# Optimization experiments

Measured on AMD Instinct MI355X. Metric: run time of the kernel, lower is better.

The kernel has to match this reference:

```python
import jax, jax.numpy as jnp
import numpy as np

B, N, QD = 2, 4096, 1024
CD = 1024
H, DH = 8, 64
INNER = H * DH  # 512


def setup_inputs() -> dict:
    key = jax.random.key(0)
    ks = jax.random.split(key, 10)
    s = lambda d: (1.0 / np.sqrt(d)).astype(np.float32)
    return {
        "x": jax.random.normal(ks[0], (B, N, QD), dtype=jnp.float32),
        "context": jax.random.normal(ks[1], (B, N, CD), dtype=jnp.float32),
        "mask": jax.random.randint(ks[2], (B, N + 1), 0, 2) > 0,
        # weights stored as [in, out] (y = x @ W), matching torch Linear math
        "Wq": jax.random.normal(ks[3], (QD, INNER), dtype=jnp.float32) * s(QD),
        "Wk": jax.random.normal(ks[4], (CD, INNER), dtype=jnp.float32) * s(CD),
        "Wv": jax.random.normal(ks[5], (CD, INNER), dtype=jnp.float32) * s(CD),
        "Wk_bg": jax.random.normal(ks[6], (QD, INNER), dtype=jnp.float32) * s(QD),
        "Wv_bg": jax.random.normal(ks[7], (QD, INNER), dtype=jnp.float32) * s(QD),
        "Wout": jax.random.normal(ks[8], (INNER, QD), dtype=jnp.float32) * s(INNER),
        "b_out": jax.random.normal(ks[9], (QD,), dtype=jnp.float32) * 0.01,
    }


def reference(x, context, mask, Wq, Wk, Wv, Wk_bg, Wv_bg, Wout, b_out):
    b, n, _ = x.shape
    scale = DH ** -0.5

    q = x @ Wq                                             # [b, n, inner]
    pooled_x = jax.lax.stop_gradient(jnp.mean(x, axis=1, keepdims=True))  # [b, 1, qd]
    k = jnp.concatenate([context @ Wk, pooled_x @ Wk_bg], axis=1)  # [b, n+1, inner]
    v = jnp.concatenate([context @ Wv, pooled_x @ Wv_bg], axis=1)  # [b, n+1, inner]

    split = lambda t: t.reshape(b, t.shape[1], H, DH).transpose(0, 2, 1, 3)  # b h j d
    qh, kh, vh = split(q), split(k), split(v)

    sim = jnp.einsum('bhid,bhjd->bhij', qh, kh) * scale     # [b, h, n, n+1]
    neg = -jnp.finfo(sim.dtype).max
    sim = jnp.where(mask[:, None, None, :], sim, neg)
    attn = jax.nn.softmax(sim, axis=-1)
    out = jnp.einsum('bhij,bhjd->bhid', attn, vh)           # [b, h, n, d]
    out = out.transpose(0, 2, 1, 3).reshape(b, n, INNER)    # [b, n, inner]
    return out @ Wout + b_out                                # dropout p=0 -> identity
```

## Files before the change

### kernel.cpp

```cpp
#include <hip/hip_runtime.h>
#include <stdint.h>

#define N_TOK 4096
#define QDIM  1024
#define CDIM  1024
#define NH    8
#define DH    64
#define INNER 512
#define BATCH 2
#define N1    4097
#define N1P   4128
#define NJB   129
#define VROWS 80
#define KTILE_SH 2048
#define VTILE_SH 2560

typedef __attribute__((ext_vector_type(8))) short short8;
typedef __attribute__((ext_vector_type(4))) float f32x4;
typedef __attribute__((ext_vector_type(4))) uint32_t u32x4;

__device__ __forceinline__ short f2bf(float f) {
    union { float f; uint32_t u; } x; x.f = f;
    uint32_t r = x.u + 0x7fffu + ((x.u >> 16) & 1u);
    return (short)(r >> 16);
}

__device__ __forceinline__ void async_copy16(void* lds, const void* g) {
    __builtin_amdgcn_global_load_lds(
        (const __attribute__((address_space(1))) void*)g,
        (__attribute__((address_space(3))) void*)lds, 16, 0, 0);
}

__global__ __launch_bounds__(256) void cast2_bf16_kernel(
        const float* __restrict__ a, const float* __restrict__ b,
        short* __restrict__ da, short* __restrict__ db, int n4) {
    int i = blockIdx.x * 256 + threadIdx.x;
    bool first = i < n4;
    const float* s = first ? a : b;
    short* d = first ? da : db;
    int j = first ? i : i - n4;
    float4 v = ((const float4*)s)[j];
    ((short4*)d)[j] = make_short4(f2bf(v.x), f2bf(v.y), f2bf(v.z), f2bf(v.w));
}

__global__ __launch_bounds__(256) void transpose_cast4_kernel(
        const float* __restrict__ Wq, const float* __restrict__ Wk,
        const float* __restrict__ Wv, const float* __restrict__ Wout,
        short* __restrict__ Wqt, short* __restrict__ Wkvt, short* __restrict__ Wot,
        float scale_q) {
    __shared__ float tile[32][33];
    int z = blockIdx.y;
    const float* W; short* Wt; int K, N; float scale = 1.f;
    if (z == 0)      { W = Wq;   Wt = Wqt;  K = QDIM;  N = INNER; scale = scale_q; }
    else if (z == 1) { W = Wk;   Wt = Wkvt; K = CDIM;  N = INNER; }
    else if (z == 2) { W = Wv;   Wt = Wkvt + (size_t)INNER * CDIM; K = CDIM; N = INNER; }
    else             { W = Wout; Wt = Wot;  K = INNER; N = QDIM; }
    int ntn = N >> 5;
    int bid = blockIdx.x;
    int n0 = (bid & (ntn - 1)) * 32, k0 = (bid / ntn) * 32;
    int tx = threadIdx.x & 31, ty = threadIdx.x >> 5;
    for (int r = ty; r < 32; r += 8)
        tile[r][tx] = W[(size_t)(k0 + r) * N + n0 + tx];
    __syncthreads();
    for (int r = ty; r < 32; r += 8)
        Wt[(size_t)(n0 + r) * K + k0 + tx] = f2bf(tile[tx][r] * scale);
}

__global__ __launch_bounds__(256) void pool_partial_kernel(
        const float* __restrict__ x, float* __restrict__ part) {
    int b = blockIdx.y, c = blockIdx.x;
    int t = threadIdx.x;
    float s0 = 0.f, s1 = 0.f, s2 = 0.f, s3 = 0.f;
    const float* xp = x + ((size_t)b * N_TOK + c * 128) * QDIM;
    for (int n = 0; n < 128; n++) {
        const float* row = xp + (size_t)n * QDIM;
        s0 += row[t];
        s1 += row[256 + t];
        s2 += row[512 + t];
        s3 += row[768 + t];
    }
    float* pp = part + ((size_t)b * 32 + c) * QDIM;
    pp[t] = s0; pp[256 + t] = s1; pp[512 + t] = s2; pp[768 + t] = s3;
}

__global__ __launch_bounds__(256) void bg_kernel(
        const float* __restrict__ part, const float* __restrict__ Wkbg,
        const float* __restrict__ Wvbg, short* __restrict__ kb, short* __restrict__ vb) {
    int b = blockIdx.x, jb = blockIdx.y, t = threadIdx.x;
    __shared__ float pooled[QDIM];
    for (int d = t; d < QDIM; d += 256) {
        float s = 0.f;
        for (int c = 0; c < 32; c++) s += part[((size_t)b * 32 + c) * QDIM + d];
        pooled[d] = s * (1.f / (float)N_TOK);
    }
    __syncthreads();
    int flat = jb * 256 + t;
    int matv = flat >> 9;
    int o = flat & 511;
    const float* W = matv ? Wvbg : Wkbg;
    float s = 0.f;
    for (int k = 0; k < QDIM; k++) s += pooled[k] * W[(size_t)k * INNER + o];
    int h = o >> 6, d = o & 63;
    if (matv) {
        vb[(((size_t)(b * NH + h)) * N1P + N_TOK) * DH + d] = f2bf(s);
    } else {
        kb[((size_t)(b * NH + h)) * NJB * KTILE_SH + 128 * KTILE_SH
           + (d >> 5) * 1024 + (d & 31)] = f2bf(s);
    }
    if (jb == 0) {
        for (int idx = t; idx < NH * 31 * DH; idx += 256) {
            int h2 = idx / (31 * DH);
            int r2 = idx % (31 * DH);
            int rr = 1 + r2 / DH;
            int d2 = r2 % DH;
            kb[((size_t)(b * NH + h2)) * NJB * KTILE_SH + 128 * KTILE_SH
               + (d2 >> 5) * 1024 + rr * 32 + (d2 & 31)] = 0;
        }
    }
}

__global__ __launch_bounds__(256) void transpose_v_kernel(
        const short* __restrict__ vin, short* __restrict__ vout,
        const int* __restrict__ mask) {
    __shared__ short tile[32][65];
    __shared__ int mloc[32];
    int bh = blockIdx.z, b = bh >> 3;
    int j0 = blockIdx.x * 32, jb = blockIdx.x;
    int tx = threadIdx.x & 63, ty = threadIdx.x >> 6;
    const short* src = vin + (size_t)bh * N1P * DH;
    for (int r = ty; r < 32; r += 4)
        tile[r][tx] = src[(size_t)(j0 + r) * DH + tx];
    if (threadIdx.x < 32) {
        int j = j0 + threadIdx.x;
        mloc[threadIdx.x] = (j < N1) ? mask[b * N1 + j] : 0;
    }
    __syncthreads();
    int tp = threadIdx.x & 31, dy = threadIdx.x >> 5;
    int s = (tp >> 3) * 4 + (tp & 3) + ((tp >> 2) & 1) * 16;
    bool mk = mloc[s] != 0;
    short* dst = vout + ((size_t)bh * NJB + jb) * VTILE_SH;
    for (int d = dy; d < DH; d += 8) {
        int swz = (((tp >> 3) ^ ((d >> 1) & 3)) << 3) | (tp & 7);
        dst[d * 32 + swz] = mk ? tile[s][d] : (short)0;
    }
    if (dy == 0) dst[64 * 32 + tp] = mk ? (short)0x3F80 : (short)0;
    if (dy == 1)
        for (int d = 65; d < 80; d++) dst[d * 32 + tp] = 0;
}

__global__ __launch_bounds__(256) void qkv_gemm_kernel(
        const short* __restrict__ x_bf, const short* __restrict__ c_bf,
        const short* __restrict__ Wqt, const short* __restrict__ Wkvt,
        short* __restrict__ q_bf, short* __restrict__ k_bf, short* __restrict__ v_tmp) {
    __shared__ short As[128 * 32];
    __shared__ short Bs[128 * 32];
    const int t = threadIdx.x;
    const int lane = t & 63, w = t >> 6;
    const int wr = w >> 1, wc = w & 1;
    const int lo = lane & 15, g = lane >> 4;
    const int arow = lane >> 2;
    const int ac8 = (lane & 3) * 8;

    const short *A, *W;
    int m0, n0, which;
    int bid = blockIdx.x;
    if (bid < 256) { A = x_bf; W = Wqt;  m0 = (bid >> 2) * 128; n0 = (bid & 3) * 128; which = 0; }
    else { int i = bid - 256; A = c_bf; W = Wkvt; m0 = (i >> 3) * 128; n0 = (i & 7) * 128;
           which = (n0 < 512) ? 1 : 2; }

    f32x4 acc[4][4] = {};
    for (int k0 = 0; k0 < 1024; k0 += 32) {
        for (int q = 0; q < 2; q++) {
            int seg = w * 2 + q;
            async_copy16(&As[seg * 512], A + (size_t)(m0 + seg * 16 + arow) * 1024 + k0 + ac8);
            async_copy16(&Bs[seg * 512], W + (size_t)(n0 + seg * 16 + arow) * 1024 + k0 + ac8);
        }
        __syncthreads();
        short8 af[4], bfv[4];
        #pragma unroll
        for (int i = 0; i < 4; i++)
            af[i] = *(const short8*)&As[(wr * 64 + i * 16 + lo) * 32 + g * 8];
        #pragma unroll
        for (int j = 0; j < 4; j++)
            bfv[j] = *(const short8*)&Bs[(wc * 64 + j * 16 + lo) * 32 + g * 8];
        #pragma unroll
        for (int i = 0; i < 4; i++)
            #pragma unroll
            for (int j = 0; j < 4; j++)
                acc[i][j] = __builtin_amdgcn_mfma_f32_16x16x32_bf16(af[i], bfv[j], acc[i][j], 0, 0, 0);
        __syncthreads();
    }

    if (which == 0) {
        #pragma unroll
        for (int i = 0; i < 4; i++)
            #pragma unroll
            for (int j = 0; j < 4; j++) {
                int row = m0 + wr * 64 + i * 16 + g * 4;
                int col0 = n0 + wc * 64 + j * 16 + lo;
                int h = col0 >> 6, d = col0 & 63;
                f32x4 v = acc[i][j];
                #pragma unroll
                for (int r = 0; r < 4; r++) {
                    int m = row + r;
                    int b = m >> 12, ii = m & 4095;
                    q_bf[(((size_t)(b * NH + h)) * N_TOK + ii) * DH + d] = f2bf(v[r]);
                }
            }
    } else if (which == 1) {
        #pragma unroll
        for (int i = 0; i < 4; i++)
            #pragma unroll
            for (int j = 0; j < 4; j++) {
                int row = m0 + wr * 64 + i * 16 + g * 4;
                int col0 = n0 + wc * 64 + j * 16 + lo;
                int h = col0 >> 6, d = col0 & 63;
                f32x4 v = acc[i][j];
                #pragma unroll
                for (int r = 0; r < 4; r++) {
                    int m = row + r;
                    int b = m >> 12, ii = m & 4095;
                    int off = (d >> 5) * 1024 + (ii & 31) * 32 + (d & 31);
                    off ^= ((ii >> 1) & 3) << 3;
                    k_bf[((size_t)(b * NH + h)) * NJB * KTILE_SH + (ii >> 5) * KTILE_SH
                         + off] = f2bf(v[r]);
                }
            }
    } else {
        #pragma unroll
        for (int i = 0; i < 4; i++)
            #pragma unroll
            for (int j = 0; j < 4; j++) {
                int row = m0 + wr * 64 + i * 16 + g * 4;
                int col0 = n0 + wc * 64 + j * 16 + lo;
                int col = col0 - 512;
                int h = col >> 6, d = col & 63;
                f32x4 v = acc[i][j];
                #pragma unroll
                for (int r = 0; r < 4; r++) {
                    int m = row + r;
                    int b = m >> 12, ii = m & 4095;
                    v_tmp[(((size_t)(b * NH + h)) * N1P + ii) * DH + d] = f2bf(v[r]);
                }
            }
    }
}

__global__ __launch_bounds__(256) void out_gemm_kernel(
        const short* __restrict__ A, const short* __restrict__ Wt,
        float* __restrict__ outf, const float* __restrict__ bias) {
    __shared__ short As[128 * 32];
    __shared__ short Bs[128 * 32];
    const int t = threadIdx.x;
    const int lane = t & 63, w = t >> 6;
    const int wr = w >> 1, wc = w & 1;
    const int lo = lane & 15, g = lane >> 4;
    const int arow = lane >> 2;
    const int ac8 = (lane & 3) * 8;
    const int m0 = blockIdx.x * 128, n0 = blockIdx.y * 128;

    f32x4 acc[4][4] = {};
    for (int k0 = 0; k0 < INNER; k0 += 32) {
        for (int q = 0; q < 2; q++) {
            int seg = w * 2 + q;
            async_copy16(&As[seg * 512], A + (size_t)(m0 + seg * 16 + arow) * INNER + k0 + ac8);
            async_copy16(&Bs[seg * 512], Wt + (size_t)(n0 + seg * 16 + arow) * INNER + k0 + ac8);
        }
        __syncthreads();
        short8 af[4], bfv[4];
        #pragma unroll
        for (int i = 0; i < 4; i++)
            af[i] = *(const short8*)&As[(wr * 64 + i * 16 + lo) * 32 + g * 8];
        #pragma unroll
        for (int j = 0; j < 4; j++)
            bfv[j] = *(const short8*)&Bs[(wc * 64 + j * 16 + lo) * 32 + g * 8];
        #pragma unroll
        for (int i = 0; i < 4; i++)
            #pragma unroll
            for (int j = 0; j < 4; j++)
                acc[i][j] = __builtin_amdgcn_mfma_f32_16x16x32_bf16(af[i], bfv[j], acc[i][j], 0, 0, 0);
        __syncthreads();
    }
    #pragma unroll
    for (int i = 0; i < 4; i++)
        #pragma unroll
        for (int j = 0; j < 4; j++) {
            int row = m0 + wr * 64 + i * 16 + g * 4;
            int col = n0 + wc * 64 + j * 16 + lo;
            f32x4 v = acc[i][j];
            #pragma unroll
            for (int r = 0; r < 4; r++)
                outf[(size_t)(row + r) * QDIM + col] = v[r] + bias[col];
        }
}

__global__ __launch_bounds__(256, 2) void attn_kernel(
        const short* __restrict__ qb,
        const short* __restrict__ kb,
        const short* __restrict__ vtb,
        short* __restrict__ ob) {
    const int t = threadIdx.x, lane = t & 63, w = t >> 6;
    const int lo = lane & 15, g = lane >> 4;
    const int gs = g ^ ((lo >> 1) & 3);
    const int id = blockIdx.x;
    const int h = id & 7, b = (id >> 3) & 1, qt = id >> 4;
    const int q0 = qt * 128 + w * 32;
    const size_t bh = (size_t)(b * NH + h);

    const short* qp = qb + (bh * N_TOK + q0 + lo) * DH;
    short8 qa[2][2];
    qa[0][0] = *(const short8*)(qp + g * 8);
    qa[0][1] = *(const short8*)(qp + 32 + g * 8);
    qa[1][0] = *(const short8*)(qp + 16 * DH + g * 8);
    qa[1][1] = *(const short8*)(qp + 16 * DH + 32 + g * 8);

    __shared__ short Kl[2][KTILE_SH];
    __shared__ short Vl[2][VTILE_SH];

    const short* ksrc = kb + bh * (size_t)NJB * KTILE_SH + w * 512 + lane * 8;
    const short* vsrc = vtb + bh * (size_t)NJB * VTILE_SH + w * 512 + lane * 8;

    f32x4 o[2][5] = {};
    f32x4 z = {};

    async_copy16(&Kl[0][w * 512], ksrc);
    async_copy16(&Vl[0][w * 512], vsrc);
    if (w == 0) async_copy16(&Vl[0][2048], vsrc + 2048);
    __syncthreads();

    for (int jb = 0; jb < NJB; ++jb) {
        const int cur = jb & 1;
        if (jb + 1 < NJB) {
            const short* ks = ksrc + (size_t)(jb + 1) * KTILE_SH;
            const short* vs = vsrc + (size_t)(jb + 1) * VTILE_SH;
            async_copy16(&Kl[cur ^ 1][w * 512], ks);
            async_copy16(&Vl[cur ^ 1][w * 512], vs);
            if (w == 0) async_copy16(&Vl[cur ^ 1][2048], vs + 2048);
        }
        const short* kl = &Kl[cur][0];
        short8 kf00 = *(const short8*)&kl[(lo) * 32 + gs * 8];
        short8 kf01 = *(const short8*)&kl[1024 + (lo) * 32 + gs * 8];
        short8 kf10 = *(const short8*)&kl[(16 + lo) * 32 + gs * 8];
        short8 kf11 = *(const short8*)&kl[1024 + (16 + lo) * 32 + gs * 8];
        const short* vl = &Vl[cur][0];
        short8 vfr[5];
        #pragma unroll
        for (int f = 0; f < 5; f++)
            vfr[f] = *(const short8*)&vl[(f * 16 + lo) * 32 + gs * 8];
        #pragma unroll
        for (int rg = 0; rg < 2; rg++) {
            f32x4 s0 = __builtin_amdgcn_mfma_f32_16x16x32_bf16(kf00, qa[rg][0], z, 0, 0, 0);
            s0 = __builtin_amdgcn_mfma_f32_16x16x32_bf16(kf01, qa[rg][1], s0, 0, 0, 0);
            f32x4 s1 = __builtin_amdgcn_mfma_f32_16x16x32_bf16(kf10, qa[rg][0], z, 0, 0, 0);
            s1 = __builtin_amdgcn_mfma_f32_16x16x32_bf16(kf11, qa[rg][1], s1, 0, 0, 0);
            uint32_t u0 = __float_as_uint(__builtin_amdgcn_exp2f(s0[0])) + 0x8000u;
            uint32_t u1 = __float_as_uint(__builtin_amdgcn_exp2f(s0[1])) + 0x8000u;
            uint32_t u2 = __float_as_uint(__builtin_amdgcn_exp2f(s0[2])) + 0x8000u;
            uint32_t u3 = __float_as_uint(__builtin_amdgcn_exp2f(s0[3])) + 0x8000u;
            uint32_t u4 = __float_as_uint(__builtin_amdgcn_exp2f(s1[0])) + 0x8000u;
            uint32_t u5 = __float_as_uint(__builtin_amdgcn_exp2f(s1[1])) + 0x8000u;
            uint32_t u6 = __float_as_uint(__builtin_amdgcn_exp2f(s1[2])) + 0x8000u;
            uint32_t u7 = __float_as_uint(__builtin_amdgcn_exp2f(s1[3])) + 0x8000u;
            u32x4 pr;
            pr[0] = __builtin_amdgcn_perm(u1, u0, 0x07060302u);
            pr[1] = __builtin_amdgcn_perm(u3, u2, 0x07060302u);
            pr[2] = __builtin_amdgcn_perm(u5, u4, 0x07060302u);
            pr[3] = __builtin_amdgcn_perm(u7, u6, 0x07060302u);
            short8 pa = __builtin_bit_cast(short8, pr);
            #pragma unroll
            for (int f = 0; f < 5; f++)
                o[rg][f] = __builtin_amdgcn_mfma_f32_16x16x32_bf16(pa, vfr[f], o[rg][f], 0, 0, 0);
        }
        __syncthreads();
    }

    short* op = ob + ((size_t)(b * N_TOK) + q0) * INNER + h * DH;
    #pragma unroll
    for (int rg = 0; rg < 2; rg++)
        #pragma unroll
        for (int r = 0; r < 4; r++) {
            float l = __shfl(o[rg][4][r], lane & 48);
            float inv = (l > 0.f) ? 1.f / l : 0.f;
            short* o_ = op + (size_t)(rg * 16 + g * 4 + r) * INNER;
            o_[lo]      = f2bf(o[rg][0][r] * inv);
            o_[16 + lo] = f2bf(o[rg][1][r] * inv);
            o_[32 + lo] = f2bf(o[rg][2][r] * inv);
            o_[48 + lo] = f2bf(o[rg][3][r] * inv);
        }
}

extern "C" void kernel_launch(void* const* d_in, const int* in_sizes, int n_in,
                              void* d_out, int out_size, void* d_ws, size_t ws_size,
                              hipStream_t stream) {
    const float* x    = (const float*)d_in[0];
    const float* ctx  = (const float*)d_in[1];
    const int*   mask = (const int*)d_in[2];
    const float* Wq   = (const float*)d_in[3];
    const float* Wk   = (const float*)d_in[4];
    const float* Wv   = (const float*)d_in[5];
    const float* Wkbg = (const float*)d_in[6];
    const float* Wvbg = (const float*)d_in[7];
    const float* Wout = (const float*)d_in[8];
    const float* bout = (const float*)d_in[9];
    float* out = (float*)d_out;

    char* p = (char*)d_ws;
    auto alloc = [&](size_t b) { char* r = p; p += (b + 255) & ~(size_t)255; return r; };
    short* x_bf  = (short*)alloc((size_t)BATCH * N_TOK * QDIM * 2);
    short* c_bf  = (short*)alloc((size_t)BATCH * N_TOK * CDIM * 2);
    short* Wqt   = (short*)alloc((size_t)INNER * QDIM * 2);
    short* Wkvt  = (short*)alloc((size_t)2 * INNER * CDIM * 2);
    short* Wot   = (short*)alloc((size_t)QDIM * INNER * 2);
    short* q_bf  = (short*)alloc((size_t)BATCH * NH * N_TOK * DH * 2);
    short* k_bf  = (short*)alloc((size_t)BATCH * NH * NJB * KTILE_SH * 2);
    short* v_tmp = (short*)alloc((size_t)BATCH * NH * N1P * DH * 2);
    short* vt_bf = (short*)alloc((size_t)BATCH * NH * NJB * VTILE_SH * 2);
    short* o_bf  = (short*)alloc((size_t)BATCH * N_TOK * INNER * 2);
    float* part  = (float*)alloc((size_t)BATCH * 32 * QDIM * 4);

    const float SCALE_Q = 0.125f * 1.4426950408889634f;

    int n4 = BATCH * N_TOK * QDIM / 4;
    cast2_bf16_kernel<<<(2 * n4 + 255) / 256, 256, 0, stream>>>(x, ctx, x_bf, c_bf, n4);

    transpose_cast4_kernel<<<dim3(512, 4), 256, 0, stream>>>(
        Wq, Wk, Wv, Wout, Wqt, Wkvt, Wot, SCALE_Q);

    pool_partial_kernel<<<dim3(32, BATCH), 256, 0, stream>>>(x, part);

    qkv_gemm_kernel<<<768, 256, 0, stream>>>(x_bf, c_bf, Wqt, Wkvt, q_bf, k_bf, v_tmp);

    bg_kernel<<<dim3(BATCH, 4), 256, 0, stream>>>(part, Wkbg, Wvbg, k_bf, v_tmp);
    transpose_v_kernel<<<dim3(NJB, 1, BATCH * NH), 256, 0, stream>>>(v_tmp, vt_bf, mask);

    attn_kernel<<<512, 256, 0, stream>>>(q_bf, k_bf, vt_bf, o_bf);

    out_gemm_kernel<<<dim3(64, 8), 256, 0, stream>>>(o_bf, Wot, out, bout);
}
```

Before: 337.4 us.

## Process two K/V tiles per pipeline stage in attention and swizzle QKV GEMM blocks

The attention loop now loads and processes two 32-key tiles per double-buffered stage. K and V are padded to 130 tiles, with the extra tile zeroed or masked, so the stage count is even. This halves the number of barriers and widens the prefetch window. The loop also wraps the MFMA sections in s_setprio. Separately, the QKV GEMM remaps block indices so blocks that run at the same time spread across the different tiles. The cost is double the LDS use per block, which may lower occupancy.

Result: faster. 319.3 us (-5.4%).

```diff
diff --git a/kernel.cpp b/kernel.cpp
--- a/kernel.cpp
+++ b/kernel.cpp
@@ -11,6 +11,7 @@
 #define N1    4097
 #define N1P   4128
 #define NJB   129
+#define NJBP  130
 #define VROWS 80
 #define KTILE_SH 2048
 #define VTILE_SH 2560
@@ -104,7 +105,7 @@
     if (matv) {
         vb[(((size_t)(b * NH + h)) * N1P + N_TOK) * DH + d] = f2bf(s);
     } else {
-        kb[((size_t)(b * NH + h)) * NJB * KTILE_SH + 128 * KTILE_SH
+        kb[((size_t)(b * NH + h)) * NJBP * KTILE_SH + 128 * KTILE_SH
            + (d >> 5) * 1024 + (d & 31)] = f2bf(s);
     }
     if (jb == 0) {
@@ -113,8 +114,13 @@
             int r2 = idx % (31 * DH);
             int rr = 1 + r2 / DH;
             int d2 = r2 % DH;
-            kb[((size_t)(b * NH + h2)) * NJB * KTILE_SH + 128 * KTILE_SH
+            kb[((size_t)(b * NH + h2)) * NJBP * KTILE_SH + 128 * KTILE_SH
                + (d2 >> 5) * 1024 + rr * 32 + (d2 & 31)] = 0;
+        }
+        for (int idx = t; idx < NH * KTILE_SH; idx += 256) {
+            int h2 = idx >> 11;
+            int off = idx & (KTILE_SH - 1);
+            kb[((size_t)(b * NH + h2)) * NJBP * KTILE_SH + 129 * KTILE_SH + off] = 0;
         }
     }
 }
@@ -128,8 +134,10 @@
     int j0 = blockIdx.x * 32, jb = blockIdx.x;
     int tx = threadIdx.x & 63, ty = threadIdx.x >> 6;
     const short* src = vin + (size_t)bh * N1P * DH;
-    for (int r = ty; r < 32; r += 4)
-        tile[r][tx] = src[(size_t)(j0 + r) * DH + tx];
+    if (j0 < N1P) {
+        for (int r = ty; r < 32; r += 4)
+            tile[r][tx] = src[(size_t)(j0 + r) * DH + tx];
+    }
     if (threadIdx.x < 32) {
         int j = j0 + threadIdx.x;
         mloc[threadIdx.x] = (j < N1) ? mask[b * N1 + j] : 0;
@@ -138,7 +146,7 @@
     int tp = threadIdx.x & 31, dy = threadIdx.x >> 5;
     int s = (tp >> 3) * 4 + (tp & 3) + ((tp >> 2) & 1) * 16;
     bool mk = mloc[s] != 0;
-    short* dst = vout + ((size_t)bh * NJB + jb) * VTILE_SH;
+    short* dst = vout + ((size_t)bh * NJBP + jb) * VTILE_SH;
     for (int d = dy; d < DH; d += 8) {
         int swz = (((tp >> 3) ^ ((d >> 1) & 3)) << 3) | (tp & 7);
         dst[d * 32 + swz] = mk ? tile[s][d] : (short)0;
@@ -163,7 +171,7 @@
 
     const short *A, *W;
     int m0, n0, which;
-    int bid = blockIdx.x;
+    int bid = (blockIdx.x & 7) * 96 + (blockIdx.x >> 3);
     if (bid < 256) { A = x_bf; W = Wqt;  m0 = (bid >> 2) * 128; n0 = (bid & 3) * 128; which = 0; }
     else { int i = bid - 256; A = c_bf; W = Wkvt; m0 = (i >> 3) * 128; n0 = (i & 7) * 128;
            which = (n0 < 512) ? 1 : 2; }
@@ -222,7 +230,7 @@
                     int b = m >> 12, ii = m & 4095;
                     int off = (d >> 5) * 1024 + (ii & 31) * 32 + (d & 31);
                     off ^= ((ii >> 1) & 3) << 3;
-                    k_bf[((size_t)(b * NH + h)) * NJB * KTILE_SH + (ii >> 5) * KTILE_SH
+                    k_bf[((size_t)(b * NH + h)) * NJBP * KTILE_SH + (ii >> 5) * KTILE_SH
                          + off] = f2bf(v[r]);
                 }
             }
@@ -314,62 +322,77 @@
     qa[1][0] = *(const short8*)(qp + 16 * DH + g * 8);
     qa[1][1] = *(const short8*)(qp + 16 * DH + 32 + g * 8);
 
-    __shared__ short Kl[2][KTILE_SH];
-    __shared__ short Vl[2][VTILE_SH];
-
-    const short* ksrc = kb + bh * (size_t)NJB * KTILE_SH + w * 512 + lane * 8;
-    const short* vsrc = vtb + bh * (size_t)NJB * VTILE_SH + w * 512 + lane * 8;
+    __shared__ short Kl[2][2][KTILE_SH];
+    __shared__ short Vl[2][2][VTILE_SH];
+
+    const short* ksrc = kb + bh * (size_t)NJBP * KTILE_SH + w * 512 + lane * 8;
+    const short* vsrc = vtb + bh * (size_t)NJBP * VTILE_SH + w * 512 + lane * 8;
 
     f32x4 o[2][5] = {};
     f32x4 z = {};
 
-    async_copy16(&Kl[0][w * 512], ksrc);
-    async_copy16(&Vl[0][w * 512], vsrc);
-    if (w == 0) async_copy16(&Vl[0][2048], vsrc + 2048);
+    async_copy16(&Kl[0][0][w * 512], ksrc);
+    async_copy16(&Vl[0][0][w * 512], vsrc);
+    async_copy16(&Kl[0][1][w * 512], ksrc + KTILE_SH);
+    async_copy16(&Vl[0][1][w * 512], vsrc + VTILE_SH);
+    if (w == 0) {
+        async_copy16(&Vl[0][0][2048], vsrc + 2048);
+        async_copy16(&Vl[0][1][2048], vsrc + VTILE_SH + 2048);
+    }
     __syncthreads();
 
-    for (int jb = 0; jb < NJB; ++jb) {
-        const int cur = jb & 1;
-        if (jb + 1 < NJB) {
-            const short* ks = ksrc + (size_t)(jb + 1) * KTILE_SH;
-            const short* vs = vsrc + (size_t)(jb + 1) * VTILE_SH;
-            async_copy16(&Kl[cur ^ 1][w * 512], ks);
-            async_copy16(&Vl[cur ^ 1][w * 512], vs);
-            if (w == 0) async_copy16(&Vl[cur ^ 1][2048], vs + 2048);
-        }
-        const short* kl = &Kl[cur][0];
-        short8 kf00 = *(const short8*)&kl[(lo) * 32 + gs * 8];
-        short8 kf01 = *(const short8*)&kl[1024 + (lo) * 32 + gs * 8];
-        short8 kf10 = *(const short8*)&kl[(16 + lo) * 32 + gs * 8];
-        short8 kf11 = *(const short8*)&kl[1024 + (16 + lo) * 32 + gs * 8];
-        const short* vl = &Vl[cur][0];
-        short8 vfr[5];
-        #pragma unroll
-        for (int f = 0; f < 5; f++)
-            vfr[f] = *(const short8*)&vl[(f * 16 + lo) * 32 + gs * 8];
-        #pragma unroll
-        for (int rg = 0; rg < 2; rg++) {
-            f32x4 s0 = __builtin_amdgcn_mfma_f32_16x16x32_bf16(kf00, qa[rg][0], z, 0, 0, 0);
-            s0 = __builtin_amdgcn_mfma_f32_16x16x32_bf16(kf01, qa[rg][1], s0, 0, 0, 0);
-            f32x4 s1 = __builtin_amdgcn_mfma_f32_16x16x32_bf16(kf10, qa[rg][0], z, 0, 0, 0);
-            s1 = __builtin_amdgcn_mfma_f32_16x16x32_bf16(kf11, qa[rg][1], s1, 0, 0, 0);
-            uint32_t u0 = __float_as_uint(__builtin_amdgcn_exp2f(s0[0])) + 0x8000u;
-            uint32_t u1 = __float_as_uint(__builtin_amdgcn_exp2f(s0[1])) + 0x8000u;
-            uint32_t u2 = __float_as_uint(__builtin_amdgcn_exp2f(s0[2])) + 0x8000u;
-            uint32_t u3 = __float_as_uint(__builtin_amdgcn_exp2f(s0[3])) + 0x8000u;
-            uint32_t u4 = __float_as_uint(__builtin_amdgcn_exp2f(s1[0])) + 0x8000u;
-            uint32_t u5 = __float_as_uint(__builtin_amdgcn_exp2f(s1[1])) + 0x8000u;
-            uint32_t u6 = __float_as_uint(__builtin_amdgcn_exp2f(s1[2])) + 0x8000u;
-            uint32_t u7 = __float_as_uint(__builtin_amdgcn_exp2f(s1[3])) + 0x8000u;
-            u32x4 pr;
-            pr[0] = __builtin_amdgcn_perm(u1, u0, 0x07060302u);
-            pr[1] = __builtin_amdgcn_perm(u3, u2, 0x07060302u);
-            pr[2] = __builtin_amdgcn_perm(u5, u4, 0x07060302u);
-            pr[3] = __builtin_amdgcn_perm(u7, u6, 0x07060302u);
-            short8 pa = __builtin_bit_cast(short8, pr);
+    for (int it = 0; it < 65; ++it) {
+        const int cur = it & 1;
+        if (it < 64) {
+            const short* ks = ksrc + (size_t)(2 * it + 2) * KTILE_SH;
+            const short* vs = vsrc + (size_t)(2 * it + 2) * VTILE_SH;
+            async_copy16(&Kl[cur ^ 1][0][w * 512], ks);
+            async_copy16(&Vl[cur ^ 1][0][w * 512], vs);
+            async_copy16(&Kl[cur ^ 1][1][w * 512], ks + KTILE_SH);
+            async_copy16(&Vl[cur ^ 1][1][w * 512], vs + VTILE_SH);
+            if (w == 0) {
+                async_copy16(&Vl[cur ^ 1][0][2048], vs + 2048);
+                async_copy16(&Vl[cur ^ 1][1][2048], vs + VTILE_SH + 2048);
+            }
+        }
+        #pragma unroll
+        for (int sub = 0; sub < 2; ++sub) {
+            const short* kl = &Kl[cur][sub][0];
+            const short* vl = &Vl[cur][sub][0];
+            __builtin_amdgcn_s_setprio(1);
+            short8 kf00 = *(const short8*)&kl[(lo) * 32 + gs * 8];
+            short8 kf01 = *(const short8*)&kl[1024 + (lo) * 32 + gs * 8];
+            short8 kf10 = *(const short8*)&kl[(16 + lo) * 32 + gs * 8];
+            short8 kf11 = *(const short8*)&kl[1024 + (16 + lo) * 32 + gs * 8];
+            short8 vfr[5];
             #pragma unroll
             for (int f = 0; f < 5; f++)
-                o[rg][f] = __builtin_amdgcn_mfma_f32_16x16x32_bf16(pa, vfr[f], o[rg][f], 0, 0, 0);
+                vfr[f] = *(const short8*)&vl[(f * 16 + lo) * 32 + gs * 8];
+            #pragma unroll
+            for (int rg = 0; rg < 2; rg++) {
+                f32x4 s0 = __builtin_amdgcn_mfma_f32_16x16x32_bf16(kf00, qa[rg][0], z, 0, 0, 0);
+                s0 = __builtin_amdgcn_mfma_f32_16x16x32_bf16(kf01, qa[rg][1], s0, 0, 0, 0);
+                f32x4 s1 = __builtin_amdgcn_mfma_f32_16x16x32_bf16(kf10, qa[rg][0], z, 0, 0, 0);
+                s1 = __builtin_amdgcn_mfma_f32_16x16x32_bf16(kf11, qa[rg][1], s1, 0, 0, 0);
+                uint32_t u0 = __float_as_uint(__builtin_amdgcn_exp2f(s0[0])) + 0x8000u;
+                uint32_t u1 = __float_as_uint(__builtin_amdgcn_exp2f(s0[1])) + 0x8000u;
+                uint32_t u2 = __float_as_uint(__builtin_amdgcn_exp2f(s0[2])) + 0x8000u;
+                uint32_t u3 = __float_as_uint(__builtin_amdgcn_exp2f(s0[3])) + 0x8000u;
+                uint32_t u4 = __float_as_uint(__builtin_amdgcn_exp2f(s1[0])) + 0x8000u;
+                uint32_t u5 = __float_as_uint(__builtin_amdgcn_exp2f(s1[1])) + 0x8000u;
+                uint32_t u6 = __float_as_uint(__builtin_amdgcn_exp2f(s1[2])) + 0x8000u;
+                uint32_t u7 = __float_as_uint(__builtin_amdgcn_exp2f(s1[3])) + 0x8000u;
+                u32x4 pr;
+                pr[0] = __builtin_amdgcn_perm(u1, u0, 0x07060302u);
+                pr[1] = __builtin_amdgcn_perm(u3, u2, 0x07060302u);
+                pr[2] = __builtin_amdgcn_perm(u5, u4, 0x07060302u);
+                pr[3] = __builtin_amdgcn_perm(u7, u6, 0x07060302u);
+                short8 pa = __builtin_bit_cast(short8, pr);
+                #pragma unroll
+                for (int f = 0; f < 5; f++)
+                    o[rg][f] = __builtin_amdgcn_mfma_f32_16x16x32_bf16(pa, vfr[f], o[rg][f], 0, 0, 0);
+            }
+            __builtin_amdgcn_s_setprio(0);
         }
         __syncthreads();
     }
@@ -412,9 +435,9 @@
     short* Wkvt  = (short*)alloc((size_t)2 * INNER * CDIM * 2);
     short* Wot   = (short*)alloc((size_t)QDIM * INNER * 2);
     short* q_bf  = (short*)alloc((size_t)BATCH * NH * N_TOK * DH * 2);
-    short* k_bf  = (short*)alloc((size_t)BATCH * NH * NJB * KTILE_SH * 2);
+    short* k_bf  = (short*)alloc((size_t)BATCH * NH * NJBP * KTILE_SH * 2);
     short* v_tmp = (short*)alloc((size_t)BATCH * NH * N1P * DH * 2);
-    short* vt_bf = (short*)alloc((size_t)BATCH * NH * NJB * VTILE_SH * 2);
+    short* vt_bf = (short*)alloc((size_t)BATCH * NH * NJBP * VTILE_SH * 2);
     short* o_bf  = (short*)alloc((size_t)BATCH * N_TOK * INNER * 2);
     float* part  = (float*)alloc((size_t)BATCH * 32 * QDIM * 4);
 
@@ -431,7 +454,7 @@
     qkv_gemm_kernel<<<768, 256, 0, stream>>>(x_bf, c_bf, Wqt, Wkvt, q_bf, k_bf, v_tmp);
 
     bg_kernel<<<dim3(BATCH, 4), 256, 0, stream>>>(part, Wkbg, Wvbg, k_bf, v_tmp);
-    transpose_v_kernel<<<dim3(NJB, 1, BATCH * NH), 256, 0, stream>>>(v_tmp, vt_bf, mask);
+    transpose_v_kernel<<<dim3(NJBP, 1, BATCH * NH), 256, 0, stream>>>(v_tmp, vt_bf, mask);
 
     attn_kernel<<<512, 256, 0, stream>>>(q_bf, k_bf, vt_bf, o_bf);
 
```
